# Kernel optimization log

Measured on AMD Instinct MI355X. Metric: run time of the kernel, lower is better.

The kernel has to match this reference:

```python
import jax, jax.numpy as jnp
import numpy as np

B, T, I, H, FF, C = 4096, 512, 13, 7, 512, 1


def setup_inputs() -> dict:
    key = jax.random.key(0)
    ks = jax.random.split(key, 9)
    s_ih = 1.0 / np.sqrt(H)
    return {
        "x": jax.random.normal(ks[0], (B, T, I), dtype=jnp.float32),
        # PyTorch LSTM params, gate order i,f,g,o, uniform(-1/sqrt(H), 1/sqrt(H))
        "w_ih": jax.random.uniform(ks[1], (4 * H, I), minval=-s_ih, maxval=s_ih, dtype=jnp.float32),
        "w_hh": jax.random.uniform(ks[2], (4 * H, H), minval=-s_ih, maxval=s_ih, dtype=jnp.float32),
        "b_ih": jax.random.uniform(ks[3], (4 * H,), minval=-s_ih, maxval=s_ih, dtype=jnp.float32),
        "b_hh": jax.random.uniform(ks[4], (4 * H,), minval=-s_ih, maxval=s_ih, dtype=jnp.float32),
        "fc1_w": jax.random.uniform(ks[5], (FF, H), minval=-s_ih, maxval=s_ih, dtype=jnp.float32),
        "fc1_b": jax.random.uniform(ks[6], (FF,), minval=-s_ih, maxval=s_ih, dtype=jnp.float32),
        "fc_w": jax.random.uniform(ks[7], (C, FF), minval=-1.0 / np.sqrt(FF), maxval=1.0 / np.sqrt(FF), dtype=jnp.float32),
        "fc_b": jax.random.uniform(ks[8], (C,), minval=-1.0 / np.sqrt(FF), maxval=1.0 / np.sqrt(FF), dtype=jnp.float32),
    }


def _lstm_last_hidden(x, w_ih, w_hh, b_ih, b_hh):
    # Precompute input contributions for all timesteps: [B, T, 4H]
    xg = jnp.einsum("bti,gi->btg", x, w_ih) + b_ih

    def step(carry, xg_t):
        h, c = carry
        gates = xg_t + h @ w_hh.T + b_hh  # [B, 4H]
        i, f, g, o = jnp.split(gates, 4, axis=-1)
        i = jax.nn.sigmoid(i)
        f = jax.nn.sigmoid(f)
        g = jnp.tanh(g)
        o = jax.nn.sigmoid(o)
        c = f * c + i * g
        h = o * jnp.tanh(c)
        return (h, c), None

    h0 = jnp.zeros((x.shape[0], w_hh.shape[1]), dtype=x.dtype)
    (hn, _), _ = jax.lax.scan(step, (h0, h0), jnp.swapaxes(xg, 0, 1))
    return hn  # [B, H]


def reference(x, w_ih, w_hh, b_ih, b_hh, fc1_w, fc1_b, fc_w, fc_b):
    # Dropout(0.1) is identity in eval mode.
    hn = _lstm_last_hidden(x, w_ih, w_hh, b_ih, b_hh)
    out = jax.nn.relu(hn)
    out = jax.nn.relu(out @ fc1_w.T + fc1_b)
    return out @ fc_w.T + fc_b  # [B, 1]
```

## Files before the change

kernel.cpp:

```cpp
#include <hip/hip_runtime.h>

#define BB 4096
#define TN 512
#define IN 13
#define HN 7
#define FFD 512
#define CT 32
#define NCK (TN / CT)
#define GPB 2

#if defined(__has_builtin)
#  if __has_builtin(__builtin_amdgcn_permlane16_swap)
#    define HAVE_PL16 1
#  endif
#endif

#define QB(v, q)    __int_as_float(__builtin_amdgcn_mov_dpp(__float_as_int(v), (q)*0x55, 0xF, 0xF, true))
#define RORF(v, n)  __int_as_float(__builtin_amdgcn_mov_dpp(__float_as_int(v), 0x120 + (n), 0xF, 0xF, true))

__device__ __forceinline__ void rowswap(float& a, float& b) {
#ifdef HAVE_PL16
    auto r = __builtin_amdgcn_permlane16_swap(__float_as_uint(a), __float_as_uint(b),
                                              false, false);
    a = __uint_as_float(r[0]);
    b = __uint_as_float(r[1]);
#else
    float ta, tb;
    asm volatile("v_mov_b32 %0, %2\n"
                 "v_mov_b32 %1, %3\n"
                 "s_nop 1\n"
                 "v_permlane16_swap_b32 %0, %1"
                 : "=&v"(ta), "=&v"(tb)
                 : "v"(a), "v"(b));
    a = ta; b = tb;
#endif
}

__device__ __forceinline__ float2 pkfma(float2 a, float2 b, float2 c) {
    float2 d;
    asm("v_pk_fma_f32 %0, %1, %2, %3" : "=v"(d) : "v"(a), "v"(b), "v"(c));
    return d;
}

__global__ __launch_bounds__(128, 4)
void lstm_fused(const float* __restrict__ x,
                const float* __restrict__ w_ih,
                const float* __restrict__ w_hh,
                const float* __restrict__ b_ih,
                const float* __restrict__ b_hh,
                const float* __restrict__ fc1_w,
                const float* __restrict__ fc1_b,
                const float* __restrict__ fc_w,
                const float* __restrict__ fc_b,
                float* __restrict__ out)
{
    __shared__ float2 xd2[2][CT/2][64];
    __shared__ float  xs[IN][GPB][CT];

    const int tid  = threadIdx.x;
    const int wid  = tid >> 6;
    const int l64  = tid & 63;
    const int grp  = l64 >> 5;
    const int lane = l64 & 31;
    const int b    = blockIdx.x * GPB + grp;

    const int tau = lane & 3;
    const int ju  = lane >> 2;
    const int jj  = (ju < HN) ? ju : (HN - 1);
    const int row = tau * HN + jj;
    const int jr  = ju & 3;

    const float L2E  = 1.4426950408889634f;
    const bool  is_tanh = (tau == 2);
    const float kmul = is_tanh ? (-2.0f * L2E) : (-L2E);
    const float sc   = is_tanh ?  2.0f : 1.0f;
    const float offc = is_tanh ? -1.0f : 0.0f;

    const int pr = __builtin_amdgcn_mov_dpp(l64, 0x124, 0xF, 0xF, true);
    const bool ror_plus = ((pr & 15) == ((l64 + 4) & 15));
    float paf = __int_as_float(l64);
    float pbf = __int_as_float(l64 + 64);
    rowswap(paf, pbf);
    const int pa = __float_as_int(paf) & 63;
    const bool a_even = (((pa >> 4) & 1) == 0);

    float2 w2[IN];
    float2 bias2;
    float  p[IN];
    const float* xbase = x + (long)b * TN * IN;

    float2 wA01, wA23, wB01, wB23;

    if (wid == 1) {
#pragma unroll
        for (int i = 0; i < IN; ++i) {
            const float w = kmul * w_ih[row * IN + i];
            w2[i] = make_float2(w, w);
        }
        const float bsum = kmul * (b_ih[row] + b_hh[row]);
        bias2 = make_float2(bsum, bsum);
    } else {
        float wA[4], wB[4];
#pragma unroll
        for (int k = 0; k < 4; ++k) {
            const int dk  = ror_plus ? k : ((4 - k) & 3);
            const int cL  = (jr + dk) & 3;
            const int cH  = 4 + ((jr + dk) & 3);
            const float wL = kmul * w_hh[row * HN + cL];
            const float wH = (cH < HN) ? kmul * w_hh[row * HN + cH] : 0.0f;
            wA[k] = a_even ? wL : wH;
            wB[k] = a_even ? wH : wL;
        }
        wA01 = make_float2(wA[0], wA[1]);
        wA23 = make_float2(wA[2], wA[3]);
        wB01 = make_float2(wB[0], wB[1]);
        wB23 = make_float2(wB[2], wB[3]);
        __builtin_amdgcn_s_setprio(1);
    }

    float2 A01 = make_float2(0.f, 0.f), A23 = make_float2(0.f, 0.f);
    float2 B01 = make_float2(0.f, 0.f), B23 = make_float2(0.f, 0.f);
    float cval = 0.0f;

#define LOADP(ck) do {                                                        \
        const float* _s = xbase + (long)((ck) * CT + lane) * IN;              \
        _Pragma("unroll")                                                     \
        for (int _i = 0; _i < IN; ++_i) p[_i] = _s[_i];                       \
    } while (0)
#define COMMITP() do {                                                        \
        _Pragma("unroll")                                                     \
        for (int _i = 0; _i < IN; ++_i) xs[_i][grp][lane] = p[_i];            \
    } while (0)
#define PROJECT(ck) do {                                                      \
        const int _buf = (ck) & 1;                                            \
        _Pragma("unroll")                                                     \
        for (int _q = 0; _q < CT; _q += 4) {                                  \
            float2 _aA = bias2, _aB = bias2;                                  \
            _Pragma("unroll")                                                 \
            for (int _i = 0; _i < IN; ++_i) {                                 \
                const float4 _xv = *(const float4*)&xs[_i][grp][_q];          \
                _aA = pkfma(w2[_i], make_float2(_xv.x, _xv.y), _aA);          \
                _aB = pkfma(w2[_i], make_float2(_xv.z, _xv.w), _aB);          \
            }                                                                 \
            xd2[_buf][(_q >> 1) + 0][l64] = _aA;                              \
            xd2[_buf][(_q >> 1) + 1][l64] = _aB;                              \
        }                                                                     \
    } while (0)

    if (wid == 1) {
        LOADP(0);
        COMMITP();
        LOADP(1);
        PROJECT(0);
    }
    __syncthreads();

    for (int ck = 0; ck < NCK; ++ck) {
        if (wid == 1) {
            const int nk = ck + 1;
            if (nk < NCK) {
                COMMITP();
                if (nk + 1 < NCK) LOADP(nk + 1);
                PROJECT(nk);
            }
        } else {
            const int buf = ck & 1;
            float2 xr2[CT / 2];
#pragma unroll
            for (int pq = 0; pq < CT / 2; ++pq) xr2[pq] = xd2[buf][pq][l64];

#pragma unroll
            for (int s = 0; s < CT; ++s) {
                const float xr = (s & 1) ? xr2[s >> 1].y : xr2[s >> 1].x;
                float2 t = pkfma(wA01, A01, make_float2(0.f, 0.f));
                t = pkfma(wA23, A23, t);
                t = pkfma(wB01, B01, t);
                t = pkfma(wB23, B23, t);
                const float sg = (t.x + t.y) + xr;

                float e   = __builtin_amdgcn_exp2f(sg);
                float val = fmaf(__builtin_amdgcn_rcpf(1.0f + e), sc, offc);

                const float iv = QB(val, 0);
                const float fv = QB(val, 1);
                const float gv = QB(val, 2);
                const float ov = QB(val, 3);

                cval = fmaf(fv, cval, iv * gv);
                float e2 = __builtin_amdgcn_exp2f(-2.0f * L2E * cval);
                float th = fmaf(__builtin_amdgcn_rcpf(1.0f + e2), 2.0f, -1.0f);
                const float hq = ov * th;

                float aa = hq, bb = hq;
                rowswap(aa, bb);
                A01.x = aa;           B01.x = bb;
                A01.y = RORF(aa, 4);  B01.y = RORF(bb, 4);
                A23.x = RORF(aa, 8);  B23.x = RORF(bb, 8);
                A23.y = RORF(aa, 12); B23.y = RORF(bb, 12);
            }
        }
        __syncthreads();
    }

    if (wid == 1) return;

    const float hA = a_even ? A01.x : B01.x;
    const float hB = a_even ? B01.x : A01.x;
    float hb[HN];
#pragma unroll
    for (int j = 0; j < 4; ++j) hb[j] = fmaxf(__shfl(hA, 4 * j, 32), 0.0f);
#pragma unroll
    for (int j = 0; j < 3; ++j) hb[4 + j] = fmaxf(__shfl(hB, 4 * j, 32), 0.0f);

    float acc = 0.0f;
#pragma unroll
    for (int k = 0; k < FFD / 32; ++k) {
        const int r = lane + (k << 5);
        float s = fc1_b[r];
#pragma unroll
        for (int j = 0; j < HN; ++j) s = fmaf(fc1_w[r * HN + j], hb[j], s);
        s = fmaxf(s, 0.0f);
        acc = fmaf(fc_w[r], s, acc);
    }
#pragma unroll
    for (int o = 16; o >= 1; o >>= 1) acc += __shfl_xor(acc, o, 32);
    if (lane == 0) out[b] = acc + fc_b[0];
}

extern "C" void kernel_launch(void* const* d_in, const int* in_sizes, int n_in,
                              void* d_out, int out_size, void* d_ws, size_t ws_size,
                              hipStream_t stream) {
    const float* x     = (const float*)d_in[0];
    const float* w_ih  = (const float*)d_in[1];
    const float* w_hh  = (const float*)d_in[2];
    const float* b_ih  = (const float*)d_in[3];
    const float* b_hh  = (const float*)d_in[4];
    const float* fc1_w = (const float*)d_in[5];
    const float* fc1_b = (const float*)d_in[6];
    const float* fc_w  = (const float*)d_in[7];
    const float* fc_b  = (const float*)d_in[8];
    float* out = (float*)d_out;

    dim3 grid(BB / GPB);
    dim3 block(128);
    hipLaunchKernelGGL(lstm_fused, grid, block, 0, stream,
                       x, w_ih, w_hh, b_ih, b_hh, fc1_w, fc1_b, fc_w, fc_b, out);
}
```

Before: 112.7 us.

## Interleave two independent LSTM recurrences per wave to hide step latency

Each block now handles four batch rows instead of two, so every recurrence wave runs two independent LSTM chains whose steps are interleaved. The aim is to hide the long serial dependency latency (exp, rcp, DPP and permlane chains) of a single recurrence by giving the scheduler independent work between dependent instructions. The packed-FMA gate dot product is replaced with scalar FMA chains, and the projection wave does twice the work per chunk. The grid halves and register use rises (launch bounds drop to 2 blocks per SIMD), and the setprio hint on the recurrence wave is removed.

```diff
diff --git a/kernel.cpp b/kernel.cpp
--- a/kernel.cpp
+++ b/kernel.cpp
@@ -7,7 +7,7 @@
 #define FFD 512
 #define CT 32
 #define NCK (TN / CT)
-#define GPB 2
+#define GPB 4
 
 #if defined(__has_builtin)
 #  if __has_builtin(__builtin_amdgcn_permlane16_swap)
@@ -42,7 +42,7 @@
     return d;
 }
 
-__global__ __launch_bounds__(128, 4)
+__global__ __launch_bounds__(128, 2)
 void lstm_fused(const float* __restrict__ x,
                 const float* __restrict__ w_ih,
                 const float* __restrict__ w_hh,
@@ -54,7 +54,7 @@
                 const float* __restrict__ fc_b,
                 float* __restrict__ out)
 {
-    __shared__ float2 xd2[2][CT/2][64];
+    __shared__ float2 xd2[2][2][CT/2][64];
     __shared__ float  xs[IN][GPB][CT];
 
     const int tid  = threadIdx.x;
@@ -62,7 +62,9 @@
     const int l64  = tid & 63;
     const int grp  = l64 >> 5;
     const int lane = l64 & 31;
-    const int b    = blockIdx.x * GPB + grp;
+    const int bbase = blockIdx.x * GPB;
+    const int bu = bbase + grp;
+    const int bv = bbase + 2 + grp;
 
     const int tau = lane & 3;
     const int ju  = lane >> 2;
@@ -86,10 +88,11 @@
 
     float2 w2[IN];
     float2 bias2;
-    float  p[IN];
-    const float* xbase = x + (long)b * TN * IN;
-
-    float2 wA01, wA23, wB01, wB23;
+    float  p0[IN], p1[IN];
+    const float* xu = x + (long)bu * TN * IN;
+    const float* xv = x + (long)bv * TN * IN;
+
+    float wA[4], wB[4];
 
     if (wid == 1) {
 #pragma unroll
@@ -100,7 +103,6 @@
         const float bsum = kmul * (b_ih[row] + b_hh[row]);
         bias2 = make_float2(bsum, bsum);
     } else {
-        float wA[4], wB[4];
 #pragma unroll
         for (int k = 0; k < 4; ++k) {
             const int dk  = ror_plus ? k : ((4 - k) & 3);
@@ -111,40 +113,70 @@
             wA[k] = a_even ? wL : wH;
             wB[k] = a_even ? wH : wL;
         }
-        wA01 = make_float2(wA[0], wA[1]);
-        wA23 = make_float2(wA[2], wA[3]);
-        wB01 = make_float2(wB[0], wB[1]);
-        wB23 = make_float2(wB[2], wB[3]);
-        __builtin_amdgcn_s_setprio(1);
-    }
-
-    float2 A01 = make_float2(0.f, 0.f), A23 = make_float2(0.f, 0.f);
-    float2 B01 = make_float2(0.f, 0.f), B23 = make_float2(0.f, 0.f);
-    float cval = 0.0f;
+    }
+
+    float au0=0.f, au1=0.f, au2=0.f, au3=0.f, bu0=0.f, bu1=0.f, bu2=0.f, bu3=0.f, cu=0.f;
+    float av0=0.f, av1=0.f, av2=0.f, av3=0.f, bv0=0.f, bv1=0.f, bv2=0.f, bv3=0.f, cv=0.f;
 
 #define LOADP(ck) do {                                                        \
-        const float* _s = xbase + (long)((ck) * CT + lane) * IN;              \
+        const float* _su = xu + (long)((ck) * CT + lane) * IN;                \
+        const float* _sv = xv + (long)((ck) * CT + lane) * IN;                \
         _Pragma("unroll")                                                     \
-        for (int _i = 0; _i < IN; ++_i) p[_i] = _s[_i];                       \
+        for (int _i = 0; _i < IN; ++_i) { p0[_i] = _su[_i]; p1[_i] = _sv[_i]; } \
     } while (0)
 #define COMMITP() do {                                                        \
         _Pragma("unroll")                                                     \
-        for (int _i = 0; _i < IN; ++_i) xs[_i][grp][lane] = p[_i];            \
+        for (int _i = 0; _i < IN; ++_i) {                                     \
+            xs[_i][grp][lane]     = p0[_i];                                   \
+            xs[_i][2 + grp][lane] = p1[_i];                                   \
+        }                                                                     \
     } while (0)
 #define PROJECT(ck) do {                                                      \
         const int _buf = (ck) & 1;                                            \
         _Pragma("unroll")                                                     \
-        for (int _q = 0; _q < CT; _q += 4) {                                  \
-            float2 _aA = bias2, _aB = bias2;                                  \
+        for (int _set = 0; _set < 2; ++_set) {                                \
+            const int _cs = _set * 2 + grp;                                   \
             _Pragma("unroll")                                                 \
-            for (int _i = 0; _i < IN; ++_i) {                                 \
-                const float4 _xv = *(const float4*)&xs[_i][grp][_q];          \
-                _aA = pkfma(w2[_i], make_float2(_xv.x, _xv.y), _aA);          \
-                _aB = pkfma(w2[_i], make_float2(_xv.z, _xv.w), _aB);          \
+            for (int _q = 0; _q < CT; _q += 4) {                              \
+                float2 _aA = bias2, _aB = bias2;                              \
+                _Pragma("unroll")                                             \
+                for (int _i = 0; _i < IN; ++_i) {                             \
+                    const float4 _xv = *(const float4*)&xs[_i][_cs][_q];      \
+                    _aA = pkfma(w2[_i], make_float2(_xv.x, _xv.y), _aA);      \
+                    _aB = pkfma(w2[_i], make_float2(_xv.z, _xv.w), _aB);      \
+                }                                                             \
+                xd2[_buf][_set][(_q >> 1) + 0][l64] = _aA;                    \
+                xd2[_buf][_set][(_q >> 1) + 1][l64] = _aB;                    \
             }                                                                 \
-            xd2[_buf][(_q >> 1) + 0][l64] = _aA;                              \
-            xd2[_buf][(_q >> 1) + 1][l64] = _aB;                              \
         }                                                                     \
+    } while (0)
+
+#define STEP(xr, A0, A1, A2, A3, B0, B1, B2, B3, CV) do {                     \
+        float _t0 = fmaf(wA[0], A0, (xr));                                    \
+        _t0 = fmaf(wA[1], A1, _t0);                                           \
+        _t0 = fmaf(wA[2], A2, _t0);                                           \
+        _t0 = fmaf(wA[3], A3, _t0);                                           \
+        float _t1 = wB[0] * B0;                                               \
+        _t1 = fmaf(wB[1], B1, _t1);                                           \
+        _t1 = fmaf(wB[2], B2, _t1);                                           \
+        _t1 = fmaf(wB[3], B3, _t1);                                           \
+        const float _sg = _t0 + _t1;                                          \
+        float _e   = __builtin_amdgcn_exp2f(_sg);                             \
+        float _val = fmaf(__builtin_amdgcn_rcpf(1.0f + _e), sc, offc);        \
+        const float _iv = QB(_val, 0);                                        \
+        const float _fv = QB(_val, 1);                                        \
+        const float _gv = QB(_val, 2);                                        \
+        const float _ov = QB(_val, 3);                                        \
+        CV = fmaf(_fv, CV, _iv * _gv);                                        \
+        float _e2 = __builtin_amdgcn_exp2f(-2.0f * L2E * CV);                 \
+        float _th = fmaf(__builtin_amdgcn_rcpf(1.0f + _e2), 2.0f, -1.0f);     \
+        const float _hq = _ov * _th;                                          \
+        float _aa = _hq, _bb = _hq;                                           \
+        rowswap(_aa, _bb);                                                    \
+        A0 = _aa;           B0 = _bb;                                         \
+        A1 = RORF(_aa, 4);  B1 = RORF(_bb, 4);                                \
+        A2 = RORF(_aa, 8);  B2 = RORF(_bb, 8);                                \
+        A3 = RORF(_aa, 12); B3 = RORF(_bb, 12);                               \
     } while (0)
 
     if (wid == 1) {
@@ -165,38 +197,21 @@
             }
         } else {
             const int buf = ck & 1;
-            float2 xr2[CT / 2];
-#pragma unroll
-            for (int pq = 0; pq < CT / 2; ++pq) xr2[pq] = xd2[buf][pq][l64];
-
-#pragma unroll
-            for (int s = 0; s < CT; ++s) {
-                const float xr = (s & 1) ? xr2[s >> 1].y : xr2[s >> 1].x;
-                float2 t = pkfma(wA01, A01, make_float2(0.f, 0.f));
-                t = pkfma(wA23, A23, t);
-                t = pkfma(wB01, B01, t);
-                t = pkfma(wB23, B23, t);
-                const float sg = (t.x + t.y) + xr;
-
-                float e   = __builtin_amdgcn_exp2f(sg);
-                float val = fmaf(__builtin_amdgcn_rcpf(1.0f + e), sc, offc);
-
-                const float iv = QB(val, 0);
-                const float fv = QB(val, 1);
-                const float gv = QB(val, 2);
-                const float ov = QB(val, 3);
-
-                cval = fmaf(fv, cval, iv * gv);
-                float e2 = __builtin_amdgcn_exp2f(-2.0f * L2E * cval);
-                float th = fmaf(__builtin_amdgcn_rcpf(1.0f + e2), 2.0f, -1.0f);
-                const float hq = ov * th;
-
-                float aa = hq, bb = hq;
-                rowswap(aa, bb);
-                A01.x = aa;           B01.x = bb;
-                A01.y = RORF(aa, 4);  B01.y = RORF(bb, 4);
-                A23.x = RORF(aa, 8);  B23.x = RORF(bb, 8);
-                A23.y = RORF(aa, 12); B23.y = RORF(bb, 12);
+#pragma unroll
+            for (int hb8 = 0; hb8 < CT / 8; ++hb8) {
+                float2 xru[4], xrv[4];
+#pragma unroll
+                for (int k = 0; k < 4; ++k) {
+                    xru[k] = xd2[buf][0][hb8 * 4 + k][l64];
+                    xrv[k] = xd2[buf][1][hb8 * 4 + k][l64];
+                }
+#pragma unroll
+                for (int k = 0; k < 4; ++k) {
+                    STEP(xru[k].x, au0,au1,au2,au3, bu0,bu1,bu2,bu3, cu);
+                    STEP(xrv[k].x, av0,av1,av2,av3, bv0,bv1,bv2,bv3, cv);
+                    STEP(xru[k].y, au0,au1,au2,au3, bu0,bu1,bu2,bu3, cu);
+                    STEP(xrv[k].y, av0,av1,av2,av3, bv0,bv1,bv2,bv3, cv);
+                }
             }
         }
         __syncthreads();
@@ -204,27 +219,35 @@
 
     if (wid == 1) return;
 
-    const float hA = a_even ? A01.x : B01.x;
-    const float hB = a_even ? B01.x : A01.x;
-    float hb[HN];
-#pragma unroll
-    for (int j = 0; j < 4; ++j) hb[j] = fmaxf(__shfl(hA, 4 * j, 32), 0.0f);
-#pragma unroll
-    for (int j = 0; j < 3; ++j) hb[4 + j] = fmaxf(__shfl(hB, 4 * j, 32), 0.0f);
-
-    float acc = 0.0f;
-#pragma unroll
-    for (int k = 0; k < FFD / 32; ++k) {
-        const int r = lane + (k << 5);
-        float s = fc1_b[r];
-#pragma unroll
-        for (int j = 0; j < HN; ++j) s = fmaf(fc1_w[r * HN + j], hb[j], s);
-        s = fmaxf(s, 0.0f);
-        acc = fmaf(fc_w[r], s, acc);
-    }
-#pragma unroll
-    for (int o = 16; o >= 1; o >>= 1) acc += __shfl_xor(acc, o, 32);
-    if (lane == 0) out[b] = acc + fc_b[0];
+    const float hAu = a_even ? au0 : bu0;
+    const float hBu = a_even ? bu0 : au0;
+    const float hAv = a_even ? av0 : bv0;
+    const float hBv = a_even ? bv0 : av0;
+
+#pragma unroll
+    for (int set = 0; set < 2; ++set) {
+        const float hA = set ? hAv : hAu;
+        const float hB = set ? hBv : hBu;
+        float hb[HN];
+#pragma unroll
+        for (int j = 0; j < 4; ++j) hb[j] = fmaxf(__shfl(hA, 4 * j, 32), 0.0f);
+#pragma unroll
+        for (int j = 0; j < 3; ++j) hb[4 + j] = fmaxf(__shfl(hB, 4 * j, 32), 0.0f);
+
+        float acc = 0.0f;
+#pragma unroll
+        for (int k = 0; k < FFD / 32; ++k) {
+            const int r = lane + (k << 5);
+            float s = fc1_b[r];
+#pragma unroll
+            for (int j = 0; j < HN; ++j) s = fmaf(fc1_w[r * HN + j], hb[j], s);
+            s = fmaxf(s, 0.0f);
+            acc = fmaf(fc_w[r], s, acc);
+        }
+#pragma unroll
+        for (int o = 16; o >= 1; o >>= 1) acc += __shfl_xor(acc, o, 32);
+        if (lane == 0) out[set ? bv : bu] = acc + fc_b[0];
+    }
 }
 
 extern "C" void kernel_launch(void* const* d_in, const int* in_sizes, int n_in,
```

After: 109.1 us. 3.2% less time.
